# Performance work log

Measured on AMD Instinct MI355X. Metric: run time of the kernel, lower is better.

## Reference

```python
import jax, jax.numpy as jnp
import numpy as np

B, S, H = 16, 512, 2048
NH, NKV = 16, 4
HD = H // NH  # 128


def _rope_tables(seq_len, dim, dtype):
    inv_freq = 1.0 / (10000.0 ** (jnp.arange(0, dim, 2, dtype=jnp.float32) / dim))
    t = jnp.arange(seq_len, dtype=jnp.float32)
    freqs = jnp.einsum('i,j->ij', t, inv_freq)          # [S, HD/2]
    emb = jnp.concatenate([freqs, freqs], axis=-1)       # [S, HD]
    cos = jnp.cos(emb)[None, None].astype(dtype)         # [1,1,S,HD]
    sin = jnp.sin(emb)[None, None].astype(dtype)
    return cos, sin


def _rotate_half(x):
    x1, x2 = jnp.split(x, 2, axis=-1)
    return jnp.concatenate([-x2, x1], axis=-1)


def setup_inputs() -> dict:
    key = jax.random.key(0)
    kx, kq, kk, kv, ko = jax.random.split(key, 5)
    x = jax.random.normal(kx, (B, S, H), dtype=jnp.float32)
    s = 0.02
    Wq = jax.random.normal(kq, (H, H), dtype=jnp.float32) * s
    Wk = jax.random.normal(kk, (NKV * HD, H), dtype=jnp.float32) * s
    Wv = jax.random.normal(kv, (NKV * HD, H), dtype=jnp.float32) * s
    Wo = jax.random.normal(ko, (H, H), dtype=jnp.float32) * s
    return {"x": x, "Wq": Wq, "Wk": Wk, "Wv": Wv, "Wo": Wo}


def reference(x, Wq, Wk, Wv, Wo):
    b, s, _ = x.shape
    scaling = HD ** -0.5
    # projections (torch Linear: y = x @ W.T, W is [out,in])
    q = jnp.einsum('bsh,oh->bso', x, Wq).reshape(b, s, NH, HD).transpose(0, 2, 1, 3)
    k = jnp.einsum('bsh,oh->bso', x, Wk).reshape(b, s, NKV, HD).transpose(0, 2, 1, 3)
    v = jnp.einsum('bsh,oh->bso', x, Wv).reshape(b, s, NKV, HD).transpose(0, 2, 1, 3)
    cos, sin = _rope_tables(s, HD, x.dtype)
    q = q * cos + _rotate_half(q) * sin
    k = k * cos + _rotate_half(k) * sin
    rep = NH // NKV
    k = jnp.repeat(k, rep, axis=1)  # [b, NH, s, HD]
    v = jnp.repeat(v, rep, axis=1)
    scores = jnp.einsum('bhqd,bhkd->bhqk', q, k) * scaling
    attn = jax.nn.softmax(scores, axis=-1)
    out = jnp.einsum('bhqk,bhkd->bhqd', attn, v)
    out = out.transpose(0, 2, 1, 3).reshape(b, s, H)
    return jnp.einsum('bsh,oh->bso', out, Wo)
```

## Files before the change

### kernel.cpp

```cpp
#include <hip/hip_runtime.h>
#include <stdint.h>


typedef _Float16 f16;
typedef _Float16 f16x4 __attribute__((ext_vector_type(4)));
typedef _Float16 f16x8 __attribute__((ext_vector_type(8)));
typedef float f32x4 __attribute__((ext_vector_type(4)));

#define B_   16
#define S_   512
#define H_   2048
#define NH_  16
#define NKV_ 4
#define HD_  128
#define ATT_SCALE 0.08838834764831843f
#define LOG2_10000_DIV64 0.20762050593045952f

#define AS1 __attribute__((address_space(1)))
#define AS3 __attribute__((address_space(3)))

__device__ __forceinline__ void async16(const void* g, const void* l) {
  __builtin_amdgcn_global_load_lds((const AS1 unsigned int*)(uintptr_t)g,
                                   (AS3 unsigned int*)(uintptr_t)l, 16, 0, 0);
}

__global__ __launch_bounds__(256) void cast_all(const float* __restrict__ x,
                                                const float* __restrict__ wq,
                                                const float* __restrict__ wk,
                                                const float* __restrict__ wv,
                                                const float* __restrict__ wo,
                                                f16* __restrict__ x_h,
                                                f16* __restrict__ w_h,
                                                f16* __restrict__ wo_h) {
  const int i = blockIdx.x * 256 + threadIdx.x;
  const float4* src;
  f16x4* dst;
  if (i < 4194304) {
    src = (const float4*)x + i;            dst = (f16x4*)x_h + i;
  } else if (i < 5242880) {
    int j = i - 4194304;
    src = (const float4*)wq + j;           dst = (f16x4*)w_h + j;
  } else if (i < 5505024) {
    int j = i - 5242880;
    src = (const float4*)wk + j;           dst = (f16x4*)w_h + 1048576 + j;
  } else if (i < 5767168) {
    int j = i - 5505024;
    src = (const float4*)wv + j;           dst = (f16x4*)w_h + 1310720 + j;
  } else {
    int j = i - 5767168;
    src = (const float4*)wo + j;           dst = (f16x4*)wo_h + j;
  }
  float4 v = *src;
  f16x4 o = {(f16)v.x, (f16)v.y, (f16)v.z, (f16)v.w};
  *dst = o;
}

template<int MODE>
__global__ __launch_bounds__(512, 2) void gemm256(const f16* __restrict__ A,
                                                  const f16* __restrict__ W,
                                                  f16* __restrict__ qo,
                                                  f16* __restrict__ ko,
                                                  f16* __restrict__ vto,
                                                  float* __restrict__ fout) {
  __shared__ __align__(16) f16 As[4][256 * 32];
  __shared__ __align__(16) f16 Bs[4][256 * 32];
  const int K = 2048;
  const int NT = 64;
  const int m0 = blockIdx.x * 256;
  const int n0 = blockIdx.y * 256;
  const int tid = threadIdx.x;
  const int wave = tid >> 6, lane = tid & 63;
  const int quad = lane >> 4, l15 = lane & 15;
  const int wm = wave >> 2, wn = wave & 3;

  const f16* aptr = A + (size_t)(m0 + (tid >> 2)) * K + (tid & 3) * 8;
  const f16* bptr = W + (size_t)(n0 + (tid >> 2)) * K + (tid & 3) * 8;
  const int ldst = wave * 1024;

  f32x4 acc[8][4] = {};

#pragma unroll
  for (int t = 0; t < 3; ++t) {
    const int k0 = t * 32;
    async16(aptr + k0,             (const char*)&As[t][0] + ldst);
    async16(aptr + 128 * K + k0,   (const char*)&As[t][0] + 8192 + ldst);
    async16(bptr + k0,             (const char*)&Bs[t][0] + ldst);
    async16(bptr + 128 * K + k0,   (const char*)&Bs[t][0] + 8192 + ldst);
  }
  asm volatile("s_waitcnt vmcnt(8)" ::: "memory");
  __builtin_amdgcn_s_barrier();

  for (int t = 0; t < NT; ++t) {
    const int buf = t & 3;
    const f16* Ab = &As[buf][0];
    const f16* Bb = &Bs[buf][0];
    const int sbuf = (t + 3) & 3;
    const int sk0 = (t + 3) * 32;
    f16x8 afr[4], bfr[4];

#pragma unroll
    for (int mi = 0; mi < 4; ++mi)
      afr[mi] = *reinterpret_cast<const f16x8*>(Ab + (wm * 128 + mi * 16 + l15) * 32 + quad * 8);
#pragma unroll
    for (int ni = 0; ni < 4; ++ni) {
      const int col = MODE ? ((wn >> 1) * 128 + (ni >> 1) * 64 + (wn & 1) * 32 + (ni & 1) * 16 + l15)
                           : (wn * 64 + ni * 16 + l15);
      bfr[ni] = *reinterpret_cast<const f16x8*>(Bb + col * 32 + quad * 8);
    }
    if (t + 3 < NT) {
      async16(aptr + sk0,           (const char*)&As[sbuf][0] + ldst);
      async16(aptr + 128 * K + sk0, (const char*)&As[sbuf][0] + 8192 + ldst);
    }
    __builtin_amdgcn_s_barrier();
    asm volatile("s_waitcnt lgkmcnt(0)" ::: "memory");
    __builtin_amdgcn_sched_barrier(0);
    __builtin_amdgcn_s_setprio(1);
#pragma unroll
    for (int mi = 0; mi < 4; ++mi)
#pragma unroll
      for (int ni = 0; ni < 4; ++ni)
        acc[mi][ni] = __builtin_amdgcn_mfma_f32_16x16x32_f16(afr[mi], bfr[ni], acc[mi][ni], 0, 0, 0);
    __builtin_amdgcn_s_setprio(0);
    __builtin_amdgcn_s_barrier();

#pragma unroll
    for (int mi = 0; mi < 4; ++mi)
      afr[mi] = *reinterpret_cast<const f16x8*>(Ab + (wm * 128 + (mi + 4) * 16 + l15) * 32 + quad * 8);
    if (t + 3 < NT) {
      async16(bptr + sk0,           (const char*)&Bs[sbuf][0] + ldst);
      async16(bptr + 128 * K + sk0, (const char*)&Bs[sbuf][0] + 8192 + ldst);
    }
    __builtin_amdgcn_s_barrier();
    asm volatile("s_waitcnt lgkmcnt(0)" ::: "memory");
    __builtin_amdgcn_sched_barrier(0);
    __builtin_amdgcn_s_setprio(1);
#pragma unroll
    for (int mi = 0; mi < 4; ++mi)
#pragma unroll
      for (int ni = 0; ni < 4; ++ni)
        acc[mi + 4][ni] = __builtin_amdgcn_mfma_f32_16x16x32_f16(afr[mi], bfr[ni], acc[mi + 4][ni], 0, 0, 0);
    __builtin_amdgcn_s_setprio(0);

    if (t + 3 < NT)      asm volatile("s_waitcnt vmcnt(8)" ::: "memory");
    else if (t + 2 < NT) asm volatile("s_waitcnt vmcnt(4)" ::: "memory");
    else if (t + 1 < NT) asm volatile("s_waitcnt vmcnt(0)" ::: "memory");
    __builtin_amdgcn_s_barrier();
  }

  if constexpr (MODE == 1) {
    const int b_ = m0 >> 9;
    if (n0 >= 2560) {
      const int h = ((n0 - 2560) >> 7) + (wn >> 1);
      f16* vb = vto + ((size_t)b_ * NKV_ + h) * HD_ * S_;
#pragma unroll
      for (int mi = 0; mi < 8; ++mi)
#pragma unroll
        for (int r = 0; r < 4; ++r) {
          const int s = (m0 + wm * 128 + mi * 16 + quad * 4 + r) & 511;
#pragma unroll
          for (int ni = 0; ni < 4; ++ni) {
            const int d = (ni >> 1) * 64 + (wn & 1) * 32 + (ni & 1) * 16 + l15;
            vb[(size_t)d * S_ + s] = (f16)acc[mi][ni][r];
          }
        }
    } else {
      f16* ob = (n0 < 2048)
          ? (qo + ((size_t)b_ * NH_ + (n0 >> 7) + (wn >> 1)) * S_ * HD_)
          : (ko + ((size_t)b_ * NKV_ + ((n0 - 2048) >> 7) + (wn >> 1)) * S_ * HD_);
      float invf[2];
#pragma unroll
      for (int ni = 0; ni < 2; ++ni)
        invf[ni] = exp2f((float)((wn & 1) * 32 + ni * 16 + l15) * -LOG2_10000_DIV64);
#pragma unroll
      for (int mi = 0; mi < 8; ++mi)
#pragma unroll
        for (int r = 0; r < 4; ++r) {
          const int s = (m0 + wm * 128 + mi * 16 + quad * 4 + r) & 511;
          const size_t rb = (size_t)s * HD_;
#pragma unroll
          for (int ni = 0; ni < 2; ++ni) {
            const int d = (wn & 1) * 32 + ni * 16 + l15;
            float sn, cs;
            __sincosf((float)s * invf[ni], &sn, &cs);
            const float x1 = acc[mi][ni][r], x2 = acc[mi][ni + 2][r];
            ob[rb + d] = (f16)(x1 * cs - x2 * sn);
            ob[rb + d + 64] = (f16)(x2 * cs + x1 * sn);
          }
        }
    }
  } else {
#pragma unroll
    for (int mi = 0; mi < 8; ++mi)
#pragma unroll
      for (int ni = 0; ni < 4; ++ni) {
        const int ncol = n0 + wn * 64 + ni * 16 + l15;
#pragma unroll
        for (int r = 0; r < 4; ++r) {
          const int mrow = m0 + wm * 128 + mi * 16 + quad * 4 + r;
          fout[(size_t)mrow * 2048 + ncol] = acc[mi][ni][r];
        }
      }
  }
}

__global__ __launch_bounds__(512) void attn_kernel(const f16* __restrict__ q,
                                                   const f16* __restrict__ k,
                                                   const f16* __restrict__ vt,
                                                   f16* __restrict__ out) {
  __shared__ __align__(16) f16 Qs[128 * 128];
  __shared__ __align__(16) f16 Ks[128 * 128];
  __shared__ __align__(16) f16 Vs[128 * 128];
  __shared__ __align__(16) f16 Ps[8][16 * 136];

  const int qt = blockIdx.x, h = blockIdx.y, b = blockIdx.z;
  const int kvh = h >> 2;
  const int tid = threadIdx.x;
  const int wave = tid >> 6, lane = tid & 63;
  const int quad = lane >> 4, l15 = lane & 15;
  const int sm0 = wave * 16;

  const f16* qbase = q + (((size_t)b * NH_ + h) * S_ + qt * 128) * HD_;
  const f16* kbase = k + ((size_t)b * NKV_ + kvh) * S_ * HD_;
  const f16* vbase = vt + ((size_t)b * NKV_ + kvh) * HD_ * S_;

#pragma unroll
  for (int i = 0; i < 4; ++i) {
    const int L = wave * 256 + i * 64 + lane;
    const int r = L >> 4;
    const int c = (L & 15) ^ (r & 15);
    async16(qbase + (size_t)r * HD_ + c * 8, (const char*)Qs + (size_t)(wave * 256 + i * 64) * 16);
  }

  f32x4 O[8] = {};
  float mrun[4], lrun[4];
#pragma unroll
  for (int r = 0; r < 4; ++r) { mrun[r] = -3.0e38f; lrun[r] = 0.f; }

  for (int j = 0; j < 4; ++j) {
    if (j) __syncthreads();
#pragma unroll
    for (int i = 0; i < 4; ++i) {
      const int L = wave * 256 + i * 64 + lane;
      const int r = L >> 4;
      const int c = (L & 15) ^ (r & 15);
      async16(kbase + (size_t)(j * 128 + r) * HD_ + c * 8,
              (const char*)Ks + (size_t)(wave * 256 + i * 64) * 16);
      async16(vbase + (size_t)r * S_ + j * 128 + c * 8,
              (const char*)Vs + (size_t)(wave * 256 + i * 64) * 16);
    }
    __syncthreads();

    f32x4 Sc[8] = {};
#pragma unroll
    for (int ks = 0; ks < 4; ++ks) {
      f16x8 aq, bk[8];
      aq = *reinterpret_cast<const f16x8*>(Qs + ((sm0 + l15) * 16 + (((ks * 4 + quad) ^ l15))) * 8);
#pragma unroll
      for (int ni = 0; ni < 8; ++ni)
        bk[ni] = *reinterpret_cast<const f16x8*>(Ks + ((ni * 16 + l15) * 16 + ((ks * 4 + quad) ^ l15)) * 8);
#pragma unroll
      for (int ni = 0; ni < 8; ++ni)
        Sc[ni] = __builtin_amdgcn_mfma_f32_16x16x32_f16(aq, bk[ni], Sc[ni], 0, 0, 0);
    }

#pragma unroll
    for (int r = 0; r < 4; ++r) {
      float mx = -3.0e38f;
#pragma unroll
      for (int ni = 0; ni < 8; ++ni) mx = fmaxf(mx, Sc[ni][r]);
      mx *= ATT_SCALE;
#pragma unroll
      for (int off = 1; off < 16; off <<= 1) mx = fmaxf(mx, __shfl_xor(mx, off));
      const float mnew = fmaxf(mrun[r], mx);
      const float alpha = __expf(mrun[r] - mnew);
      float rs = 0.f;
#pragma unroll
      for (int ni = 0; ni < 8; ++ni) {
        const float pv = __expf(Sc[ni][r] * ATT_SCALE - mnew);
        Sc[ni][r] = pv;
        rs += pv;
      }
#pragma unroll
      for (int off = 1; off < 16; off <<= 1) rs += __shfl_xor(rs, off);
      lrun[r] = lrun[r] * alpha + rs;
      mrun[r] = mnew;
#pragma unroll
      for (int ni = 0; ni < 8; ++ni) O[ni][r] *= alpha;
#pragma unroll
      for (int ni = 0; ni < 8; ++ni)
        Ps[wave][(quad * 4 + r) * 136 + ni * 16 + l15] = (f16)Sc[ni][r];
    }

#pragma unroll
    for (int ks = 0; ks < 4; ++ks) {
      f16x8 ap, bv[8];
      ap = *reinterpret_cast<const f16x8*>(&Ps[wave][l15 * 136 + ks * 32 + quad * 8]);
#pragma unroll
      for (int ni = 0; ni < 8; ++ni)
        bv[ni] = *reinterpret_cast<const f16x8*>(Vs + ((ni * 16 + l15) * 16 + ((ks * 4 + quad) ^ l15)) * 8);
#pragma unroll
      for (int ni = 0; ni < 8; ++ni)
        O[ni] = __builtin_amdgcn_mfma_f32_16x16x32_f16(ap, bv[ni], O[ni], 0, 0, 0);
    }
  }

#pragma unroll
  for (int r = 0; r < 4; ++r) {
    const float inv = 1.f / lrun[r];
    const int srow = qt * 128 + sm0 + quad * 4 + r;
#pragma unroll
    for (int ni = 0; ni < 8; ++ni)
      out[((size_t)b * S_ + srow) * H_ + h * HD_ + ni * 16 + l15] = (f16)(O[ni][r] * inv);
  }
}

extern "C" void kernel_launch(void* const* d_in, const int* in_sizes, int n_in,
                              void* d_out, int out_size, void* d_ws, size_t ws_size,
                              hipStream_t stream) {
  const float* x = (const float*)d_in[0];
  const float* Wq = (const float*)d_in[1];
  const float* Wk = (const float*)d_in[2];
  const float* Wv = (const float*)d_in[3];
  const float* Wo = (const float*)d_in[4];
  float* out = (float*)d_out;
  char* ws = (char*)d_ws;

  f16* x_h  = (f16*)(ws + 0);
  f16* w_h  = (f16*)(ws + 33554432);
  f16* wo_h = (f16*)(ws + 46137344);
  f16* qb   = (f16*)(ws + 54525952);
  f16* kb   = (f16*)(ws + 88080384);
  f16* vtb  = (f16*)(ws + 96468992);
  f16* attn = (f16*)(ws + 104857600);

  cast_all<<<26624, 256, 0, stream>>>(x, Wq, Wk, Wv, Wo, x_h, w_h, wo_h);
  gemm256<1><<<dim3(32, 12), 512, 0, stream>>>(x_h, w_h, qb, kb, vtb, nullptr);
  attn_kernel<<<dim3(4, 16, 16), 512, 0, stream>>>(qb, kb, vtb, attn);
  gemm256<0><<<dim3(32, 8), 512, 0, stream>>>(attn, wo_h, nullptr, nullptr, nullptr, out);
}
```

Before: 427.2 us.

## Restructure GEMM to 256x128 tiles with BK=64, XOR-swizzled LDS, register double-buffering

Rewrites the projection GEMM kernel to use 256x128 output tiles with a K-step of 64, a triple-buffered LDS ring and an XOR swizzle on LDS slots to avoid bank conflicts. LDS fragments for the next half-step are loaded into registers while the current MFMAs run, which cuts the barriers per iteration. Block counts double (768 and 512 blocks), which improves the fill of the 256 CUs. The cost is less A-operand reuse per tile, and therefore more global traffic, plus more complex wait-count bookkeeping.

```diff
diff --git a/kernel.cpp b/kernel.cpp
--- a/kernel.cpp
+++ b/kernel.cpp
@@ -56,130 +56,154 @@
 }
 
 template<int MODE>
-__global__ __launch_bounds__(512, 2) void gemm256(const f16* __restrict__ A,
-                                                  const f16* __restrict__ W,
-                                                  f16* __restrict__ qo,
-                                                  f16* __restrict__ ko,
-                                                  f16* __restrict__ vto,
-                                                  float* __restrict__ fout) {
-  __shared__ __align__(16) f16 As[4][256 * 32];
-  __shared__ __align__(16) f16 Bs[4][256 * 32];
+__global__ __launch_bounds__(512, 2) void gemm_k(const f16* __restrict__ A,
+                                                 const f16* __restrict__ W,
+                                                 f16* __restrict__ qo,
+                                                 f16* __restrict__ ko,
+                                                 f16* __restrict__ vto,
+                                                 float* __restrict__ fout) {
+  __shared__ __align__(16) f16 As[3][256 * 64];
+  __shared__ __align__(16) f16 Bs[3][128 * 64];
   const int K = 2048;
-  const int NT = 64;
+  const int NT = 32;
   const int m0 = blockIdx.x * 256;
-  const int n0 = blockIdx.y * 256;
+  const int n0 = blockIdx.y * 128;
   const int tid = threadIdx.x;
   const int wave = tid >> 6, lane = tid & 63;
   const int quad = lane >> 4, l15 = lane & 15;
-  const int wm = wave >> 2, wn = wave & 3;
-
-  const f16* aptr = A + (size_t)(m0 + (tid >> 2)) * K + (tid & 3) * 8;
-  const f16* bptr = W + (size_t)(n0 + (tid >> 2)) * K + (tid & 3) * 8;
-  const int ldst = wave * 1024;
-
-  f32x4 acc[8][4] = {};
-
-#pragma unroll
-  for (int t = 0; t < 3; ++t) {
-    const int k0 = t * 32;
-    async16(aptr + k0,             (const char*)&As[t][0] + ldst);
-    async16(aptr + 128 * K + k0,   (const char*)&As[t][0] + 8192 + ldst);
-    async16(bptr + k0,             (const char*)&Bs[t][0] + ldst);
-    async16(bptr + 128 * K + k0,   (const char*)&Bs[t][0] + 8192 + ldst);
-  }
-  asm volatile("s_waitcnt vmcnt(8)" ::: "memory");
+  const int wm = wave >> 1, wn = wave & 1;
+
+  const f16* aptr[4];
+  const f16* bptr[2];
+#pragma unroll
+  for (int i = 0; i < 4; ++i) {
+    const int L = i * 512 + wave * 64 + lane;
+    const int r = L >> 3, s = L & 7;
+    aptr[i] = A + (size_t)(m0 + r) * K + (s ^ (r & 7)) * 8;
+  }
+#pragma unroll
+  for (int i = 0; i < 2; ++i) {
+    const int L = i * 512 + wave * 64 + lane;
+    const int r = L >> 3, s = L & 7;
+    bptr[i] = W + (size_t)(n0 + r) * K + (s ^ (r & 7)) * 8;
+  }
+  const int ldsw = wave * 1024;
+
+  f32x4 acc[4][4] = {};
+  f16x8 aC[4], bC[4], aN[4], bN[4];
+
+  auto ldA = [&](f16x8* d, const f16* base, int ks) {
+#pragma unroll
+    for (int mi = 0; mi < 4; ++mi) {
+      const int row = wm * 64 + mi * 16 + l15;
+      const int slot = (ks * 4 + quad) ^ (l15 & 7);
+      d[mi] = *reinterpret_cast<const f16x8*>(base + row * 64 + slot * 8);
+    }
+  };
+  auto ldB = [&](f16x8* d, const f16* base, int ks) {
+#pragma unroll
+    for (int ni = 0; ni < 4; ++ni) {
+      const int col = wn * 32 + (ni >> 1) * 64 + (ni & 1) * 16 + l15;
+      const int slot = (ks * 4 + quad) ^ (l15 & 7);
+      d[ni] = *reinterpret_cast<const f16x8*>(base + col * 64 + slot * 8);
+    }
+  };
+  auto mfma16 = [&](const f16x8* Af, const f16x8* Bf) {
+#pragma unroll
+    for (int mi = 0; mi < 4; ++mi)
+#pragma unroll
+      for (int ni = 0; ni < 4; ++ni)
+        acc[mi][ni] = __builtin_amdgcn_mfma_f32_16x16x32_f16(Af[mi], Bf[ni], acc[mi][ni], 0, 0, 0);
+  };
+
+#pragma unroll
+  for (int t = 0; t < 2; ++t) {
+#pragma unroll
+    for (int i = 0; i < 4; ++i)
+      async16(aptr[i] + t * 64, (const char*)&As[t][0] + i * 8192 + ldsw);
+#pragma unroll
+    for (int i = 0; i < 2; ++i)
+      async16(bptr[i] + t * 64, (const char*)&Bs[t][0] + i * 8192 + ldsw);
+  }
+  asm volatile("s_waitcnt vmcnt(6)" ::: "memory");
   __builtin_amdgcn_s_barrier();
+  ldA(aC, &As[0][0], 0);
+  ldB(bC, &Bs[0][0], 0);
 
   for (int t = 0; t < NT; ++t) {
-    const int buf = t & 3;
-    const f16* Ab = &As[buf][0];
-    const f16* Bb = &Bs[buf][0];
-    const int sbuf = (t + 3) & 3;
-    const int sk0 = (t + 3) * 32;
-    f16x8 afr[4], bfr[4];
-
-#pragma unroll
-    for (int mi = 0; mi < 4; ++mi)
-      afr[mi] = *reinterpret_cast<const f16x8*>(Ab + (wm * 128 + mi * 16 + l15) * 32 + quad * 8);
-#pragma unroll
-    for (int ni = 0; ni < 4; ++ni) {
-      const int col = MODE ? ((wn >> 1) * 128 + (ni >> 1) * 64 + (wn & 1) * 32 + (ni & 1) * 16 + l15)
-                           : (wn * 64 + ni * 16 + l15);
-      bfr[ni] = *reinterpret_cast<const f16x8*>(Bb + col * 32 + quad * 8);
-    }
-    if (t + 3 < NT) {
-      async16(aptr + sk0,           (const char*)&As[sbuf][0] + ldst);
-      async16(aptr + 128 * K + sk0, (const char*)&As[sbuf][0] + 8192 + ldst);
-    }
-    __builtin_amdgcn_s_barrier();
-    asm volatile("s_waitcnt lgkmcnt(0)" ::: "memory");
+    const int buf = t % 3, bufn = (t + 1) % 3, bufs = (t + 2) % 3;
+    const int sk = (t + 2) * 64;
+
+    ldA(aN, &As[buf][0], 1);
+    ldB(bN, &Bs[buf][0], 1);
+    if (t + 2 < NT) {
+      async16(aptr[0] + sk, (const char*)&As[bufs][0] + 0 * 8192 + ldsw);
+      async16(aptr[1] + sk, (const char*)&As[bufs][0] + 1 * 8192 + ldsw);
+      async16(bptr[0] + sk, (const char*)&Bs[bufs][0] + 0 * 8192 + ldsw);
+    }
+    asm volatile("s_waitcnt lgkmcnt(8)" ::: "memory");
     __builtin_amdgcn_sched_barrier(0);
     __builtin_amdgcn_s_setprio(1);
-#pragma unroll
-    for (int mi = 0; mi < 4; ++mi)
-#pragma unroll
-      for (int ni = 0; ni < 4; ++ni)
-        acc[mi][ni] = __builtin_amdgcn_mfma_f32_16x16x32_f16(afr[mi], bfr[ni], acc[mi][ni], 0, 0, 0);
+    mfma16(aC, bC);
     __builtin_amdgcn_s_setprio(0);
-    __builtin_amdgcn_s_barrier();
-
-#pragma unroll
-    for (int mi = 0; mi < 4; ++mi)
-      afr[mi] = *reinterpret_cast<const f16x8*>(Ab + (wm * 128 + (mi + 4) * 16 + l15) * 32 + quad * 8);
-    if (t + 3 < NT) {
-      async16(bptr + sk0,           (const char*)&Bs[sbuf][0] + ldst);
-      async16(bptr + 128 * K + sk0, (const char*)&Bs[sbuf][0] + 8192 + ldst);
-    }
-    __builtin_amdgcn_s_barrier();
-    asm volatile("s_waitcnt lgkmcnt(0)" ::: "memory");
+
+    if (t + 1 < NT) {
+      if (t + 2 < NT) asm volatile("s_waitcnt vmcnt(3)" ::: "memory");
+      else            asm volatile("s_waitcnt vmcnt(0)" ::: "memory");
+      __builtin_amdgcn_s_barrier();
+    }
+
+    if (t + 1 < NT) {
+      ldA(aC, &As[bufn][0], 0);
+      ldB(bC, &Bs[bufn][0], 0);
+    }
+    if (t + 2 < NT) {
+      async16(aptr[2] + sk, (const char*)&As[bufs][0] + 2 * 8192 + ldsw);
+      async16(aptr[3] + sk, (const char*)&As[bufs][0] + 3 * 8192 + ldsw);
+      async16(bptr[1] + sk, (const char*)&Bs[bufs][0] + 1 * 8192 + ldsw);
+    }
+    if (t + 1 < NT) asm volatile("s_waitcnt lgkmcnt(8)" ::: "memory");
+    else            asm volatile("s_waitcnt lgkmcnt(0)" ::: "memory");
     __builtin_amdgcn_sched_barrier(0);
     __builtin_amdgcn_s_setprio(1);
-#pragma unroll
-    for (int mi = 0; mi < 4; ++mi)
-#pragma unroll
-      for (int ni = 0; ni < 4; ++ni)
-        acc[mi + 4][ni] = __builtin_amdgcn_mfma_f32_16x16x32_f16(afr[mi], bfr[ni], acc[mi + 4][ni], 0, 0, 0);
+    mfma16(aN, bN);
     __builtin_amdgcn_s_setprio(0);
-
-    if (t + 3 < NT)      asm volatile("s_waitcnt vmcnt(8)" ::: "memory");
-    else if (t + 2 < NT) asm volatile("s_waitcnt vmcnt(4)" ::: "memory");
-    else if (t + 1 < NT) asm volatile("s_waitcnt vmcnt(0)" ::: "memory");
-    __builtin_amdgcn_s_barrier();
+    if (t + 1 < NT) __builtin_amdgcn_s_barrier();
   }
 
   if constexpr (MODE == 1) {
     const int b_ = m0 >> 9;
     if (n0 >= 2560) {
-      const int h = ((n0 - 2560) >> 7) + (wn >> 1);
+      const int h = (n0 - 2560) >> 7;
       f16* vb = vto + ((size_t)b_ * NKV_ + h) * HD_ * S_;
 #pragma unroll
-      for (int mi = 0; mi < 8; ++mi)
+      for (int mi = 0; mi < 4; ++mi)
 #pragma unroll
         for (int r = 0; r < 4; ++r) {
-          const int s = (m0 + wm * 128 + mi * 16 + quad * 4 + r) & 511;
+          const int s = (m0 + wm * 64 + mi * 16 + quad * 4 + r) & 511;
 #pragma unroll
           for (int ni = 0; ni < 4; ++ni) {
-            const int d = (ni >> 1) * 64 + (wn & 1) * 32 + (ni & 1) * 16 + l15;
+            const int d = (ni >> 1) * 64 + wn * 32 + (ni & 1) * 16 + l15;
             vb[(size_t)d * S_ + s] = (f16)acc[mi][ni][r];
           }
         }
     } else {
       f16* ob = (n0 < 2048)
-          ? (qo + ((size_t)b_ * NH_ + (n0 >> 7) + (wn >> 1)) * S_ * HD_)
-          : (ko + ((size_t)b_ * NKV_ + ((n0 - 2048) >> 7) + (wn >> 1)) * S_ * HD_);
+          ? (qo + ((size_t)b_ * NH_ + (n0 >> 7)) * S_ * HD_)
+          : (ko + ((size_t)b_ * NKV_ + ((n0 - 2048) >> 7)) * S_ * HD_);
       float invf[2];
 #pragma unroll
       for (int ni = 0; ni < 2; ++ni)
-        invf[ni] = exp2f((float)((wn & 1) * 32 + ni * 16 + l15) * -LOG2_10000_DIV64);
-#pragma unroll
-      for (int mi = 0; mi < 8; ++mi)
+        invf[ni] = exp2f((float)(wn * 32 + ni * 16 + l15) * -LOG2_10000_DIV64);
+#pragma unroll
+      for (int mi = 0; mi < 4; ++mi)
 #pragma unroll
         for (int r = 0; r < 4; ++r) {
-          const int s = (m0 + wm * 128 + mi * 16 + quad * 4 + r) & 511;
+          const int s = (m0 + wm * 64 + mi * 16 + quad * 4 + r) & 511;
           const size_t rb = (size_t)s * HD_;
 #pragma unroll
           for (int ni = 0; ni < 2; ++ni) {
-            const int d = (wn & 1) * 32 + ni * 16 + l15;
+            const int d = wn * 32 + ni * 16 + l15;
             float sn, cs;
             __sincosf((float)s * invf[ni], &sn, &cs);
             const float x1 = acc[mi][ni][r], x2 = acc[mi][ni + 2][r];
@@ -190,13 +214,13 @@
     }
   } else {
 #pragma unroll
-    for (int mi = 0; mi < 8; ++mi)
+    for (int mi = 0; mi < 4; ++mi)
 #pragma unroll
       for (int ni = 0; ni < 4; ++ni) {
-        const int ncol = n0 + wn * 64 + ni * 16 + l15;
+        const int ncol = n0 + wn * 32 + (ni >> 1) * 64 + (ni & 1) * 16 + l15;
 #pragma unroll
         for (int r = 0; r < 4; ++r) {
-          const int mrow = m0 + wm * 128 + mi * 16 + quad * 4 + r;
+          const int mrow = m0 + wm * 64 + mi * 16 + quad * 4 + r;
           fout[(size_t)mrow * 2048 + ncol] = acc[mi][ni][r];
         }
       }
@@ -334,7 +358,7 @@
   f16* attn = (f16*)(ws + 104857600);
 
   cast_all<<<26624, 256, 0, stream>>>(x, Wq, Wk, Wv, Wo, x_h, w_h, wo_h);
-  gemm256<1><<<dim3(32, 12), 512, 0, stream>>>(x_h, w_h, qb, kb, vtb, nullptr);
+  gemm_k<1><<<dim3(32, 24), 512, 0, stream>>>(x_h, w_h, qb, kb, vtb, nullptr);
   attn_kernel<<<dim3(4, 16, 16), 512, 0, stream>>>(qb, kb, vtb, attn);
-  gemm256<0><<<dim3(32, 8), 512, 0, stream>>>(attn, wo_h, nullptr, nullptr, nullptr, out);
-}
+  gemm_k<0><<<dim3(32, 16), 512, 0, stream>>>(attn, wo_h, nullptr, nullptr, nullptr, out);
+}
```

After: 381.7 us. 1.12x faster.
